# Kernel tuning notes

Hardware: AMD Instinct MI355X
Metric: run time of the kernel (lower is better)

The kernel has to match this reference:

```python
import jax, jax.numpy as jnp
import numpy as np

K = 1023   # kernel_size == embedding_dim
H = 16     # out_channels (filters per sample)
E = 256    # num_embeddings
T = 8      # num_tokens
CC = 0.25  # commitment cost
EPS = np.float32(np.finfo(np.float32).eps)
DN = ('NCH', 'OIH', 'NCH')


def setup_inputs() -> dict:
    key = jax.random.key(0)
    ks = jax.random.split(key, 10)
    B, C, L = 8, 1, 8184
    D_ff = 2 * E
    X = jax.random.normal(ks[0], (B, C, L), jnp.float32)
    embedding = jax.random.uniform(ks[1], (E, K), jnp.float32, -1.0 / E, 1.0 / E)
    ffn_w1 = jax.random.normal(ks[2], (E, D_ff), jnp.float32) * 0.02
    ffn_b1 = jnp.zeros((D_ff,), jnp.float32)
    ffn_w2 = jax.random.normal(ks[3], (D_ff, E), jnp.float32) * 0.02
    ffn_b2 = jnp.zeros((E,), jnp.float32)
    ln_g = jnp.ones((E,), jnp.float32)
    ln_b = jnp.zeros((E,), jnp.float32)
    cls_w = jax.random.normal(ks[4], (E, 10), jnp.float32) * 0.02
    cls_b = jnp.zeros((10,), jnp.float32)
    return dict(X=X, embedding=embedding, ffn_w1=ffn_w1, ffn_b1=ffn_b1,
                ffn_w2=ffn_w2, ffn_b2=ffn_b2, ln_g=ln_g, ln_b=ln_b,
                cls_w=cls_w, cls_b=cls_b)


def _autocov(f):
    # f: [..., K]. FFT-based autocovariance of hann-windowed, max-normalized frame.
    n = f.shape[-1]
    fmax = jnp.max(jnp.abs(f), axis=-1, keepdims=True)
    fmax = jnp.where(fmax == 0, EPS, fmax)
    win = 0.5 * (1.0 - jnp.cos(2.0 * jnp.pi * jnp.arange(n, dtype=jnp.float32) / n))
    xw = f * win / fmax
    spec = jnp.abs(jnp.fft.rfft(xw, n=n) ** 2)   # |rfft(x)^2| == |rfft(x)|^2
    return jnp.fft.ifftshift(jnp.fft.irfft(spec, n=n), axes=-1)


def reference(X, embedding, ffn_w1, ffn_b1, ffn_w2, ffn_b2, ln_g, ln_b, cls_w, cls_b):
    B, C, L = X.shape
    # ---- encoder: extract frames at fixed linspace positions, autocovariance ----
    Lp = ((L + K - 1) // K) * K          # PadForConv(zero) length (no-op here)
    end = Lp - K - 1 - K
    positions = jnp.linspace(0.0, float(end), H).astype(jnp.int32)
    idx = positions[:, None] + jnp.arange(K)          # (H, K)
    frames = X[:, :, idx]                             # (B, C, H, K) gather
    Z = _autocov(jnp.transpose(frames, (0, 2, 1, 3)))  # (B, H, C, K)
    # ---- VQ: pairwise distances + argmin + codebook lookup ----
    flat = Z.reshape(-1, K)                           # (B*H*C, K)
    d = (jnp.sum(flat ** 2, axis=1, keepdims=True)
         + jnp.sum(embedding ** 2, axis=1)
         - 2.0 * flat @ embedding.T)                  # (B*H*C, E)
    codes = jnp.argmin(d, axis=1)
    enc = jax.nn.one_hot(codes, E, dtype=flat.dtype)
    quant = (enc @ embedding).reshape(Z.shape)
    sg = jax.lax.stop_gradient
    e_loss = jnp.mean((sg(quant) - Z) ** 2)
    q_loss = jnp.mean((quant - sg(Z)) ** 2)
    vq_loss = q_loss + CC * e_loss
    quant_st = Z + sg(quant - Z)                      # straight-through
    avg = jnp.mean(enc, axis=0)
    perplexity = jnp.exp(-jnp.sum(avg * jnp.log(avg + EPS)))
    # ---- decoder: every sample's filter bank convolved with the whole batch ----
    fmerged = quant_st.reshape(B * H, C, K)           # merge per-sample banks
    out = jax.lax.conv_general_dilated(X, fmerged, (1,), 'SAME',
                                       dimension_numbers=DN)  # (B, B*H, L)
    out = out.reshape(B, B, H, L)                     # (batch b, filter-sample i, k, L)
    sq = (out - X[:, None, :, :]) ** 2                # C==1 broadcast
    # sum_i mean_k mse_{b,l} == mean over (b,k,l) then sum over i
    recon_loss = jnp.sum(jnp.mean(sq, axis=(0, 2, 3)))
    # ---- project: conv with codebook as filters ----
    pfilt = jnp.broadcast_to(embedding[:, None, :], (E, C, K))
    proj = jax.lax.conv_general_dilated(X, pfilt, (1,), 'VALID',
                                        dimension_numbers=DN)  # (B, E, Lo)
    Lo = proj.shape[-1]
    pad = ((Lo + T - 1) // T) * T - Lo                # PadForConv(mean)
    m = jnp.mean(proj, axis=-1, keepdims=True)
    proj = jnp.concatenate([proj, jnp.broadcast_to(m, (B, E, pad))], axis=-1)
    # ---- classify ----
    x = proj.reshape(B, E, T, -1).transpose(0, 2, 3, 1)  # (B, T, t, E)
    x = jnp.max(x, axis=2)                               # (B, T, E)
    mu = jnp.mean(x, axis=-1, keepdims=True)
    var = jnp.var(x, axis=-1, keepdims=True)
    xn = (x - mu) / jnp.sqrt(var + 1e-5) * ln_g + ln_b
    hdd = jax.nn.relu(xn @ ffn_w1 + ffn_b1) @ ffn_w2 + ffn_b2
    feat = jnp.mean(hdd, axis=1)                         # (B, E)
    logits = feat @ cls_w + cls_b
    return (logits, vq_loss, recon_loss, perplexity)
```

## Files before the change

kernel.cpp:

```cpp
#include <hip/hip_runtime.h>

#define KK 1023
#define LL 8184
#define LO 7162
#define XPS 10240
#define EPSF 1.1920928955078125e-07f
#define NEG_INF (-3.4028234663852886e+38f)

typedef short bf16x8 __attribute__((ext_vector_type(8)));
typedef float f32x4 __attribute__((ext_vector_type(4)));

__device__ __constant__ int c_pos[16] = {0,409,818,1227,1636,2045,2454,2863,
                                         3273,3682,4091,4500,4909,5318,5727,6137};

__device__ __forceinline__ unsigned short f2bf(float f) {
    unsigned u = __float_as_uint(f);
    unsigned r = (u + 0x7FFFu + ((u >> 16) & 1u)) >> 16;
    return (unsigned short)r;
}
__device__ __forceinline__ int fenc(float f) {
    int u = __float_as_int(f);
    return u >= 0 ? u : (~u) ^ 0x80000000;
}
__device__ __forceinline__ float fdec(int k) {
    int u = k >= 0 ? k : ~(k ^ 0x80000000);
    return __int_as_float(u);
}
__device__ __forceinline__ void gl2lds16(const void* g, void* l) {
    __builtin_amdgcn_global_load_lds(
        (const __attribute__((address_space(1))) void*)g,
        (__attribute__((address_space(3))) void*)l, 16, 0, 0);
}

__global__ __launch_bounds__(256) void k_prep(const float* __restrict__ X,
                                              const float* __restrict__ emb,
                                              unsigned short* __restrict__ Xpad,
                                              unsigned short* __restrict__ Xodd,
                                              unsigned short* __restrict__ Ebf,
                                              float* __restrict__ Etf,
                                              float* __restrict__ enorm,
                                              int* __restrict__ hist,
                                              int* __restrict__ cmax) {
    __shared__ float red[256];
    const int q = blockIdx.x;
    const int tid = threadIdx.x;
    if (q < 32) {
        const int b = q >> 2, seg = q & 3;
        for (int i = seg * 2560 + tid; i < (seg + 1) * 2560; i += 256) {
            unsigned short v = 0, vo = 0;
            if (i >= 512 && i < 512 + LL) v = f2bf(X[b * LL + (i - 512)]);
            const int i1 = i + 1;
            if (i1 >= 512 && i1 < 512 + LL) vo = f2bf(X[b * LL + (i1 - 512)]);
            Xpad[b * XPS + i] = v;
            Xodd[b * XPS + i] = vo;
        }
    } else if (q < 288) {
        const int e = q - 32;
        const float* er = emb + e * KK;
        float nrm = 0.f;
        for (int k = tid; k < 1024; k += 256) {
            float v = (k < KK) ? er[k] : 0.f;
            Ebf[e * 1024 + k] = (k < KK) ? f2bf(v) : (unsigned short)0;
            Etf[(k >> 2) * 1024 + e * 4 + (k & 3)] = v;
            nrm = fmaf(v, v, nrm);
        }
        red[tid] = nrm;
        __syncthreads();
        for (int off = 128; off; off >>= 1) {
            if (tid < off) red[tid] += red[tid + off];
            __syncthreads();
        }
        if (tid == 0) enorm[e] = red[0];
    } else {
        const int i = (q - 288) * 256 + tid;
        cmax[i] = INT_MIN;
        if (q == 288) hist[tid] = 0;
    }
}

__global__ __launch_bounds__(256) void k_autocov(const float* __restrict__ X,
                                                 float* __restrict__ Z) {
    __shared__ __align__(16) float xw[2046];
    __shared__ float red[256];
    const int fi = blockIdx.x >> 1, half = blockIdx.x & 1;
    const int b = fi >> 4, h = fi & 15;
    const int tid = threadIdx.x;
    const float* xp = X + b * LL + c_pos[h];

    float lmax = 0.f;
    for (int j = tid; j < KK; j += 256) {
        float v = xp[j];
        xw[j] = v;
        lmax = fmaxf(lmax, fabsf(v));
    }
    red[tid] = lmax;
    __syncthreads();
    for (int off = 128; off; off >>= 1) {
        if (tid < off) red[tid] = fmaxf(red[tid], red[tid + off]);
        __syncthreads();
    }
    float fmx = red[0];
    if (fmx == 0.f) fmx = EPSF;
    __syncthreads();
    for (int j = tid; j < KK; j += 256) {
        float v = xw[j];
        float win = 0.5f * (1.0f - cosf(6.28318530717958647692f * (float)j / 1023.0f));
        float w = v * win / fmx;
        xw[j] = w;
        xw[j + KK] = w;
    }
    __syncthreads();

    const int m2 = half * 512 + 2 * tid;
    const int mh = m2 >> 1;
    const float2* X2 = (const float2*)xw;
    float a0 = 0.f, a1 = 0.f;
    float2 F = X2[mh];
#pragma unroll 4
    for (int jh = 0; jh < 511; ++jh) {
        float2 xj = X2[jh];
        float2 G = X2[mh + jh + 1];
        a0 = fmaf(xj.x, F.x, a0);
        a0 = fmaf(xj.y, F.y, a0);
        a1 = fmaf(xj.x, F.y, a1);
        a1 = fmaf(xj.y, G.x, a1);
        F = G;
    }
    float xt = xw[1022];
    a0 = fmaf(xt, F.x, a0);
    a1 = fmaf(xt, F.y, a1);
    float* zrow = Z + fi * KK;
    int i0 = m2 + 512; if (i0 >= KK) i0 -= KK;
    zrow[i0] = a0;
    if (m2 + 1 < KK) {
        int i1 = m2 + 513; if (i1 >= KK) i1 -= KK;
        zrow[i1] = a1;
    }
}

__global__ __launch_bounds__(256) void k_vq(const float* __restrict__ Z,
                                            const float4* __restrict__ Et4,
                                            const float* __restrict__ enorm,
                                            const float* __restrict__ emb,
                                            int* __restrict__ codes,
                                            int* __restrict__ hist,
                                            float* __restrict__ vq_part) {
    __shared__ float zl[KK];
    __shared__ __align__(16) float zm2[1024];
    __shared__ float rv[256];
    __shared__ int   ri[256];
    const int fi = blockIdx.x, tid = threadIdx.x;
    const float* zrow = Z + fi * KK;
    for (int t = tid; t < 1024; t += 256) {
        float z = (t < KK) ? zrow[t] : 0.f;
        if (t < KK) zl[t] = z;
        zm2[t] = -2.f * z;
    }
    __syncthreads();

    float d = enorm[tid];
    const float4* zp = (const float4*)zm2;
    const float4* ep = Et4 + tid;
#pragma unroll 8
    for (int t4 = 0; t4 < 256; ++t4) {
        float4 ev = ep[t4 * 256];
        float4 zv = zp[t4];
        d = fmaf(zv.x, ev.x, d);
        d = fmaf(zv.y, ev.y, d);
        d = fmaf(zv.z, ev.z, d);
        d = fmaf(zv.w, ev.w, d);
    }
    rv[tid] = d; ri[tid] = tid;
    __syncthreads();
    for (int off = 128; off; off >>= 1) {
        if (tid < off) {
            float v2 = rv[tid + off]; int i2 = ri[tid + off];
            if (v2 < rv[tid] || (v2 == rv[tid] && i2 < ri[tid])) { rv[tid] = v2; ri[tid] = i2; }
        }
        __syncthreads();
    }
    const int code = ri[0];
    if (tid == 0) { codes[fi] = code; atomicAdd(&hist[code], 1); }

    const float* qr = emb + code * KK;
    float s = 0.f;
    for (int t = tid; t < KK; t += 256) { float dd = qr[t] - zl[t]; s += dd * dd; }
    __syncthreads();
    rv[tid] = s;
    __syncthreads();
    for (int off = 128; off; off >>= 1) {
        if (tid < off) rv[tid] += rv[tid + off];
        __syncthreads();
    }
    if (tid == 0) vq_part[fi] = rv[0];
}

__global__ __launch_bounds__(512, 6) void k_gemm(const unsigned short* __restrict__ Xpad,
                                                 const unsigned short* __restrict__ Xodd,
                                                 const unsigned short* __restrict__ Ebf,
                                                 const int* __restrict__ codes,
                                                 const float* __restrict__ X,
                                                 float* __restrict__ psum_part,
                                                 float* __restrict__ recon_part,
                                                 int* __restrict__ cmax) {
    __shared__ __align__(16) unsigned short lds_b[8 * 1280];
    __shared__ __align__(16) unsigned short lds_a[2 * 2048];
    __shared__ float red_s[64][4];
    const int tid  = threadIdx.x;
    const int lane = tid & 63;
    const int c = lane & 15, g = lane >> 4;
    const int w = tid >> 6, we = w & 1, wg = w >> 1;

    const int bi = blockIdx.x;
    const bool isproj = bi < 1024;
    int b, l0, row0;
    if (isproj) { b = bi >> 7; int r = bi & 127; row0 = (r >> 5) * 64; l0 = (r & 31) * 256; }
    else        { int q = bi - 1024; b = q >> 6; int r = q & 63; row0 = (r >> 5) * 64; l0 = (r & 31) * 256; }
    const int xw0 = (isproj ? 512 : 0) + l0;

    {
        const unsigned short* base_e = Xpad + b * XPS + xw0;
        const unsigned short* base_o = Xodd + b * XPS + xw0;
        for (int k = tid; k < 1280; k += 512) {
            const int wdw = k / 160;
            const int p = k - wdw * 160;
            const unsigned short* src = (wdw & 1) ? (base_o + wdw - 1 + p * 8)
                                                  : (base_e + wdw + p * 8);
            gl2lds16(src, lds_b + k * 8);
        }
    }
    const unsigned short* e_src = nullptr;
    if (tid < 256) {
        const int r_lds = tid >> 2, q4 = tid & 3;
        const int grow = isproj ? (row0 + r_lds) : codes[row0 + r_lds];
        e_src = Ebf + grow * 1024 + q4 * 8;
        gl2lds16(e_src, lds_a + tid * 8);
    }
    __syncthreads();

    f32x4 acc[2][4];
#pragma unroll
    for (int i = 0; i < 2; ++i)
#pragma unroll
        for (int j = 0; j < 4; ++j) acc[i][j] = (f32x4){0.f, 0.f, 0.f, 0.f};

    const char* lax = (const char*)lds_a;
    const char* lbx = (const char*)lds_b;
    const int boff0 = (wg & 1) * 10240 + ((wg >> 1) << 4) + 32 * c + 16 * g;
    const int aoff0 = (we * 32 + c) * 64 + g * 16;

    for (int s = 0; s < 32; ++s) {
        const int cur = s & 1;
        if (s + 1 < 32 && tid < 256)
            gl2lds16(e_src + (s + 1) * 32, lds_a + ((s + 1) & 1) * 2048 + tid * 8);
        const char* ab = lax + cur * 4096 + aoff0;
        bf16x8 af0 = *(const bf16x8*)(ab);
        bf16x8 af1 = *(const bf16x8*)(ab + 1024);
#pragma unroll
        for (int ntl = 0; ntl < 4; ++ntl) {
            bf16x8 bfrag = *(const bf16x8*)(lbx + boff0 + ntl * 2560 + 64 * s);
            acc[0][ntl] = __builtin_amdgcn_mfma_f32_16x16x32_bf16(af0, bfrag, acc[0][ntl], 0, 0, 0);
            acc[1][ntl] = __builtin_amdgcn_mfma_f32_16x16x32_bf16(af1, bfrag, acc[1][ntl], 0, 0, 0);
        }
        __syncthreads();
    }

    const int lseg  = l0 >> 8;
    const int lbase = l0 + wg * 4;
    if (isproj) {
        const int ch0 = lbase / 896;
#pragma unroll
        for (int et = 0; et < 2; ++et) {
#pragma unroll
            for (int r = 0; r < 4; ++r) {
                float ssum = 0.f, m0 = NEG_INF, m1 = NEG_INF;
#pragma unroll
                for (int ntl = 0; ntl < 4; ++ntl) {
                    float v = acc[et][ntl][r];
                    int l = lbase + ntl + 16 * c;
                    bool ok = l < LO;
                    ssum += ok ? v : 0.f;
                    int ch = l / 896;
                    if (ok && ch == ch0) m0 = fmaxf(m0, v);
                    if (ok && ch != ch0) m1 = fmaxf(m1, v);
                }
                ssum += __shfl_xor(ssum, 1); ssum += __shfl_xor(ssum, 2);
                ssum += __shfl_xor(ssum, 4); ssum += __shfl_xor(ssum, 8);
                m0 = fmaxf(m0, __shfl_xor(m0, 1)); m0 = fmaxf(m0, __shfl_xor(m0, 2));
                m0 = fmaxf(m0, __shfl_xor(m0, 4)); m0 = fmaxf(m0, __shfl_xor(m0, 8));
                m1 = fmaxf(m1, __shfl_xor(m1, 1)); m1 = fmaxf(m1, __shfl_xor(m1, 2));
                m1 = fmaxf(m1, __shfl_xor(m1, 4)); m1 = fmaxf(m1, __shfl_xor(m1, 8));
                if (c == 0) {
                    int eidx = we * 32 + et * 16 + g * 4 + r;
                    red_s[eidx][wg] = ssum;
                    int e = row0 + eidx;
                    int cb = (b * 256 + e) * 8;
                    if (m0 > NEG_INF && ch0 < 8)     atomicMax(&cmax[cb + ch0], fenc(m0));
                    if (m1 > NEG_INF && ch0 + 1 < 8) atomicMax(&cmax[cb + ch0 + 1], fenc(m1));
                }
            }
        }
    } else {
        float xv[4];
#pragma unroll
        for (int ntl = 0; ntl < 4; ++ntl) {
            int lr = lbase + ntl + 16 * c - 1;
            xv[ntl] = (lr >= 0 && lr < LL) ? X[b * LL + lr] : 0.f;
        }
#pragma unroll
        for (int et = 0; et < 2; ++et) {
#pragma unroll
            for (int r = 0; r < 4; ++r) {
                float ssum = 0.f;
#pragma unroll
                for (int ntl = 0; ntl < 4; ++ntl) {
                    int lr = lbase + ntl + 16 * c - 1;
                    bool ok = (lr >= 0) && (lr < LL);
                    float dd = ok ? (acc[et][ntl][r] - xv[ntl]) : 0.f;
                    ssum += dd * dd;
                }
                ssum += __shfl_xor(ssum, 1); ssum += __shfl_xor(ssum, 2);
                ssum += __shfl_xor(ssum, 4); ssum += __shfl_xor(ssum, 8);
                if (c == 0) red_s[we * 32 + et * 16 + g * 4 + r][wg] = ssum;
            }
        }
    }
    __syncthreads();
    if (tid < 64) {
        float tot = red_s[tid][0] + red_s[tid][1] + red_s[tid][2] + red_s[tid][3];
        if (isproj) {
            int e = row0 + tid;
            psum_part[lseg * 2048 + b * 256 + e] = tot;
        } else {
            int f = row0 + tid;
            recon_part[(b * 128 + f) * 32 + lseg] = tot;
        }
    }
}

__global__ __launch_bounds__(256) void k_ln(const float* __restrict__ psum_part,
                                            const int* __restrict__ cmax,
                                            const float* __restrict__ ln_g,
                                            const float* __restrict__ ln_b,
                                            float* __restrict__ xn) {
    __shared__ float red[256];
    __shared__ float red2[256];
    const int bt = blockIdx.x;
    const int t = bt & 7;
    const int b = bt >> 3;
    const int e = threadIdx.x;
    const float* ps = psum_part + b * 256 + e;
    float sm = 0.f;
#pragma unroll
    for (int s = 0; s < 32; ++s) sm += ps[s * 2048];
    float m = sm * (1.0f / 7162.0f);
    const int cb = (b * 256 + e) << 3;
    float v = (t < 7) ? fdec(cmax[cb + t]) : fmaxf(fdec(cmax[cb + 7]), m);
    red[e] = v; red2[e] = v * v;
    __syncthreads();
    for (int off = 128; off; off >>= 1) {
        if (e < off) { red[e] += red[e + off]; red2[e] += red2[e + off]; }
        __syncthreads();
    }
    float mu  = red[0] * (1.0f / 256.0f);
    float var = red2[0] * (1.0f / 256.0f) - mu * mu;
    float r = 1.0f / sqrtf(var + 1e-5f);
    xn[bt * 256 + e] = (v - mu) * r * ln_g[e] + ln_b[e];
}

__global__ __launch_bounds__(256) void k_ffn1(const float* __restrict__ xn,
                                              const float* __restrict__ w1,
                                              const float* __restrict__ b1,
                                              float* __restrict__ hbuf) {
    __shared__ float xr[256];
    __shared__ float rv[256];
    const int q = blockIdx.x;
    const int bt = q & 63, jc = q >> 6;
    const int tid = threadIdx.x;
    xr[tid] = xn[bt * 256 + tid];
    __syncthreads();
    const int jj = tid & 63, ks = tid >> 6;
    const int j = jc * 64 + jj;
    const float* wp = w1 + (ks * 64) * 512 + j;
    float a = 0.f;
#pragma unroll
    for (int ee = 0; ee < 64; ++ee) a = fmaf(xr[ks * 64 + ee], wp[ee * 512], a);
    rv[tid] = a;
    __syncthreads();
    if (tid < 64) {
        float s = rv[tid] + rv[tid + 64] + rv[tid + 128] + rv[tid + 192];
        hbuf[bt * 512 + jc * 64 + tid] = fmaxf(s + b1[jc * 64 + tid], 0.f);
    }
}

__global__ __launch_bounds__(256) void k_ffn2(const float* __restrict__ hbuf,
                                              const float* __restrict__ w2,
                                              const float* __restrict__ b2,
                                              float* __restrict__ hdd) {
    __shared__ float hr[512];
    __shared__ float rv[256];
    const int q = blockIdx.x;
    const int bt = q & 63, jc = q >> 6;
    const int tid = threadIdx.x;
    hr[tid] = hbuf[bt * 512 + tid];
    hr[tid + 256] = hbuf[bt * 512 + 256 + tid];
    __syncthreads();
    const int jj = tid & 63, ks = tid >> 6;
    const int e = jc * 64 + jj;
    const float* wp = w2 + (ks * 128) * 256 + e;
    float a = 0.f;
#pragma unroll
    for (int j = 0; j < 128; ++j) a = fmaf(hr[ks * 128 + j], wp[j * 256], a);
    rv[tid] = a;
    __syncthreads();
    if (tid < 64) {
        float s = rv[tid] + rv[tid + 64] + rv[tid + 128] + rv[tid + 192];
        hdd[bt * 256 + jc * 64 + tid] = s + b2[jc * 64 + tid];
    }
}

__global__ __launch_bounds__(256) void k_final(const float* __restrict__ hdd,
                                               const float* __restrict__ cls_w,
                                               const float* __restrict__ cls_b,
                                               const float* __restrict__ recon_part,
                                               const float* __restrict__ vq_part,
                                               const int* __restrict__ hist,
                                               float* __restrict__ out) {
    __shared__ float red[256];
    const int tid = threadIdx.x;
    if (blockIdx.x == 0) {
        __shared__ float feat[8][256];
#pragma unroll
        for (int b2 = 0; b2 < 8; ++b2) {
            float fb = 0.f;
#pragma unroll
            for (int t2 = 0; t2 < 8; ++t2) fb += hdd[(b2 * 8 + t2) * 256 + tid];
            feat[b2][tid] = fb * 0.125f;
        }
        __syncthreads();
        if (tid < 80) {
            const int b = tid / 10, k = tid % 10;
            float a = cls_b[k];
            for (int e = 0; e < 256; ++e) a = fmaf(feat[b][e], cls_w[e * 10 + k], a);
            out[tid] = a;
        }
    } else {
        float s = 0.f;
        for (int i = tid; i < 32768; i += 256) s += recon_part[i];
        red[tid] = s;
        __syncthreads();
        for (int off = 128; off; off >>= 1) { if (tid < off) red[tid] += red[tid + off]; __syncthreads(); }
        if (tid == 0) out[81] = red[0] / 1047552.0f;
        __syncthreads();
        red[tid] = (tid < 128) ? vq_part[tid] : 0.f;
        __syncthreads();
        for (int off = 128; off; off >>= 1) { if (tid < off) red[tid] += red[tid + off]; __syncthreads(); }
        if (tid == 0) out[80] = 1.25f * red[0] / 130944.0f;
        __syncthreads();
        float avg = (float)hist[tid] * (1.0f / 128.0f);
        red[tid] = avg * logf(avg + EPSF);
        __syncthreads();
        for (int off = 128; off; off >>= 1) { if (tid < off) red[tid] += red[tid + off]; __syncthreads(); }
        if (tid == 0) out[82] = expf(-red[0]);
    }
}

extern "C" void kernel_launch(void* const* d_in, const int* in_sizes, int n_in,
                              void* d_out, int out_size, void* d_ws, size_t ws_size,
                              hipStream_t stream) {
    const float* X     = (const float*)d_in[0];
    const float* emb   = (const float*)d_in[1];
    const float* w1    = (const float*)d_in[2];
    const float* b1    = (const float*)d_in[3];
    const float* w2    = (const float*)d_in[4];
    const float* b2    = (const float*)d_in[5];
    const float* ln_g  = (const float*)d_in[6];
    const float* ln_b  = (const float*)d_in[7];
    const float* cls_w = (const float*)d_in[8];
    const float* cls_b = (const float*)d_in[9];
    float* out = (float*)d_out;

    float* Z            = (float*)d_ws;
    float* vq_part      = Z + 130944;
    float* xnbuf        = vq_part + 128;
    float* hdd          = xnbuf + 16384;
    float* psum_part    = hdd + 16384;
    float* recon_part   = psum_part + 65536;
    int*   cmaxb        = (int*)(recon_part + 32768);
    int*   codes        = cmaxb + 16384;
    int*   hist         = codes + 128;
    unsigned short* Xpad = (unsigned short*)(hist + 256);
    unsigned short* Xodd = Xpad + 8 * XPS;
    unsigned short* Ebf  = Xodd + 8 * XPS;
    float* Etf           = (float*)(Ebf + 256 * 1024);
    float* enorm         = Etf + 256 * 1024;
    float* hbuf          = enorm + 256;

    k_prep   <<<dim3(352), dim3(256), 0, stream>>>(X, emb, Xpad, Xodd, Ebf, Etf, enorm, hist, cmaxb);
    k_autocov<<<dim3(256), dim3(256), 0, stream>>>(X, Z);
    k_vq     <<<dim3(128), dim3(256), 0, stream>>>(Z, (const float4*)Etf, enorm, emb, codes, hist, vq_part);
    k_gemm   <<<dim3(1536), dim3(512), 0, stream>>>(Xpad, Xodd, Ebf, codes, X, psum_part, recon_part, cmaxb);
    k_ln     <<<dim3(64),  dim3(256), 0, stream>>>(psum_part, cmaxb, ln_g, ln_b, xnbuf);
    k_ffn1   <<<dim3(512), dim3(256), 0, stream>>>(xnbuf, w1, b1, hbuf);
    k_ffn2   <<<dim3(256), dim3(256), 0, stream>>>(hbuf, w2, b2, hdd);
    k_final  <<<dim3(2),   dim3(256), 0, stream>>>(hdd, cls_w, cls_b, recon_part, vq_part, hist, out);
}
```

Baseline: 141.9 us.

## Merge autocov into prep kernel and give GEMM waves four row tiles

```diff
diff --git a/kernel.cpp b/kernel.cpp
--- a/kernel.cpp
+++ b/kernel.cpp
@@ -32,20 +32,91 @@
         (__attribute__((address_space(3))) void*)l, 16, 0, 0);
 }
 
-__global__ __launch_bounds__(256) void k_prep(const float* __restrict__ X,
-                                              const float* __restrict__ emb,
-                                              unsigned short* __restrict__ Xpad,
-                                              unsigned short* __restrict__ Xodd,
-                                              unsigned short* __restrict__ Ebf,
-                                              float* __restrict__ Etf,
-                                              float* __restrict__ enorm,
-                                              int* __restrict__ hist,
-                                              int* __restrict__ cmax) {
+__global__ __launch_bounds__(256) void k_pa(const float* __restrict__ X,
+                                            const float* __restrict__ emb,
+                                            unsigned short* __restrict__ Xpad,
+                                            unsigned short* __restrict__ Xodd,
+                                            unsigned short* __restrict__ Ebf,
+                                            float* __restrict__ Etf,
+                                            float* __restrict__ enorm,
+                                            int* __restrict__ hist,
+                                            int* __restrict__ cmax,
+                                            float* __restrict__ Z) {
+    __shared__ __align__(16) float xw[2046];
     __shared__ float red[256];
     const int q = blockIdx.x;
     const int tid = threadIdx.x;
-    if (q < 32) {
-        const int b = q >> 2, seg = q & 3;
+    if (q < 256) {
+        const int fi = q >> 1, half = q & 1;
+        const int b = fi >> 4, h = fi & 15;
+        const float* xp = X + b * LL + c_pos[h];
+        float lmax = 0.f;
+        for (int j = tid; j < KK; j += 256) {
+            float v = xp[j];
+            xw[j] = v;
+            lmax = fmaxf(lmax, fabsf(v));
+        }
+        red[tid] = lmax;
+        __syncthreads();
+        for (int off = 128; off; off >>= 1) {
+            if (tid < off) red[tid] = fmaxf(red[tid], red[tid + off]);
+            __syncthreads();
+        }
+        float fmx = red[0];
+        if (fmx == 0.f) fmx = EPSF;
+        __syncthreads();
+        for (int j = tid; j < KK; j += 256) {
+            float v = xw[j];
+            float win = 0.5f * (1.0f - cosf(6.28318530717958647692f * (float)j / 1023.0f));
+            float w = v * win / fmx;
+            xw[j] = w;
+            xw[j + KK] = w;
+        }
+        __syncthreads();
+
+        const int m2 = half * 512 + 2 * tid;
+        const int mh = m2 >> 1;
+        const float2* X2 = (const float2*)xw;
+        float a0 = 0.f, a1 = 0.f;
+        float2 F = X2[mh];
+#pragma unroll 2
+        for (int jh = 0; jh < 510; jh += 2) {
+            float2 xj0 = X2[jh];
+            float2 xj1 = X2[jh + 1];
+            float2 G0 = X2[mh + jh + 1];
+            float2 G1 = X2[mh + jh + 2];
+            a0 = fmaf(xj0.x, F.x, a0);
+            a0 = fmaf(xj0.y, F.y, a0);
+            a1 = fmaf(xj0.x, F.y, a1);
+            a1 = fmaf(xj0.y, G0.x, a1);
+            a0 = fmaf(xj1.x, G0.x, a0);
+            a0 = fmaf(xj1.y, G0.y, a0);
+            a1 = fmaf(xj1.x, G0.y, a1);
+            a1 = fmaf(xj1.y, G1.x, a1);
+            F = G1;
+        }
+        {
+            float2 xj = X2[510];
+            float2 G = X2[mh + 511];
+            a0 = fmaf(xj.x, F.x, a0);
+            a0 = fmaf(xj.y, F.y, a0);
+            a1 = fmaf(xj.x, F.y, a1);
+            a1 = fmaf(xj.y, G.x, a1);
+            F = G;
+        }
+        float xt = xw[1022];
+        a0 = fmaf(xt, F.x, a0);
+        a1 = fmaf(xt, F.y, a1);
+        float* zrow = Z + fi * KK;
+        int i0 = m2 + 512; if (i0 >= KK) i0 -= KK;
+        zrow[i0] = a0;
+        if (m2 + 1 < KK) {
+            int i1 = m2 + 513; if (i1 >= KK) i1 -= KK;
+            zrow[i1] = a1;
+        }
+    } else if (q < 288) {
+        const int qq = q - 256;
+        const int b = qq >> 2, seg = qq & 3;
         for (int i = seg * 2560 + tid; i < (seg + 1) * 2560; i += 256) {
             unsigned short v = 0, vo = 0;
             if (i >= 512 && i < 512 + LL) v = f2bf(X[b * LL + (i - 512)]);
@@ -54,8 +125,8 @@
             Xpad[b * XPS + i] = v;
             Xodd[b * XPS + i] = vo;
         }
-    } else if (q < 288) {
-        const int e = q - 32;
+    } else if (q < 544) {
+        const int e = q - 288;
         const float* er = emb + e * KK;
         float nrm = 0.f;
         for (int k = tid; k < 1024; k += 256) {
@@ -72,69 +143,9 @@
         }
         if (tid == 0) enorm[e] = red[0];
     } else {
-        const int i = (q - 288) * 256 + tid;
+        const int i = (q - 544) * 256 + tid;
         cmax[i] = INT_MIN;
-        if (q == 288) hist[tid] = 0;
-    }
-}
-
-__global__ __launch_bounds__(256) void k_autocov(const float* __restrict__ X,
-                                                 float* __restrict__ Z) {
-    __shared__ __align__(16) float xw[2046];
-    __shared__ float red[256];
-    const int fi = blockIdx.x >> 1, half = blockIdx.x & 1;
-    const int b = fi >> 4, h = fi & 15;
-    const int tid = threadIdx.x;
-    const float* xp = X + b * LL + c_pos[h];
-
-    float lmax = 0.f;
-    for (int j = tid; j < KK; j += 256) {
-        float v = xp[j];
-        xw[j] = v;
-        lmax = fmaxf(lmax, fabsf(v));
-    }
-    red[tid] = lmax;
-    __syncthreads();
-    for (int off = 128; off; off >>= 1) {
-        if (tid < off) red[tid] = fmaxf(red[tid], red[tid + off]);
-        __syncthreads();
-    }
-    float fmx = red[0];
-    if (fmx == 0.f) fmx = EPSF;
-    __syncthreads();
-    for (int j = tid; j < KK; j += 256) {
-        float v = xw[j];
-        float win = 0.5f * (1.0f - cosf(6.28318530717958647692f * (float)j / 1023.0f));
-        float w = v * win / fmx;
-        xw[j] = w;
-        xw[j + KK] = w;
-    }
-    __syncthreads();
-
-    const int m2 = half * 512 + 2 * tid;
-    const int mh = m2 >> 1;
-    const float2* X2 = (const float2*)xw;
-    float a0 = 0.f, a1 = 0.f;
-    float2 F = X2[mh];
-#pragma unroll 4
-    for (int jh = 0; jh < 511; ++jh) {
-        float2 xj = X2[jh];
-        float2 G = X2[mh + jh + 1];
-        a0 = fmaf(xj.x, F.x, a0);
-        a0 = fmaf(xj.y, F.y, a0);
-        a1 = fmaf(xj.x, F.y, a1);
-        a1 = fmaf(xj.y, G.x, a1);
-        F = G;
-    }
-    float xt = xw[1022];
-    a0 = fmaf(xt, F.x, a0);
-    a1 = fmaf(xt, F.y, a1);
-    float* zrow = Z + fi * KK;
-    int i0 = m2 + 512; if (i0 >= KK) i0 -= KK;
-    zrow[i0] = a0;
-    if (m2 + 1 < KK) {
-        int i1 = m2 + 513; if (i1 >= KK) i1 -= KK;
-        zrow[i1] = a1;
+        if (q == 544) hist[tid] = 0;
     }
 }
 
@@ -195,7 +206,7 @@
     if (tid == 0) vq_part[fi] = rv[0];
 }
 
-__global__ __launch_bounds__(512, 6) void k_gemm(const unsigned short* __restrict__ Xpad,
+__global__ __launch_bounds__(256, 4) void k_gemm(const unsigned short* __restrict__ Xpad,
                                                  const unsigned short* __restrict__ Xodd,
                                                  const unsigned short* __restrict__ Ebf,
                                                  const int* __restrict__ codes,
@@ -209,7 +220,7 @@
     const int tid  = threadIdx.x;
     const int lane = tid & 63;
     const int c = lane & 15, g = lane >> 4;
-    const int w = tid >> 6, we = w & 1, wg = w >> 1;
+    const int wg = tid >> 6;
 
     const int bi = blockIdx.x;
     const bool isproj = bi < 1024;
@@ -221,7 +232,7 @@
     {
         const unsigned short* base_e = Xpad + b * XPS + xw0;
         const unsigned short* base_o = Xodd + b * XPS + xw0;
-        for (int k = tid; k < 1280; k += 512) {
+        for (int k = tid; k < 1280; k += 256) {
             const int wdw = k / 160;
             const int p = k - wdw * 160;
             const unsigned short* src = (wdw & 1) ? (base_o + wdw - 1 + p * 8)
@@ -229,38 +240,37 @@
             gl2lds16(src, lds_b + k * 8);
         }
     }
-    const unsigned short* e_src = nullptr;
-    if (tid < 256) {
-        const int r_lds = tid >> 2, q4 = tid & 3;
-        const int grow = isproj ? (row0 + r_lds) : codes[row0 + r_lds];
-        e_src = Ebf + grow * 1024 + q4 * 8;
-        gl2lds16(e_src, lds_a + tid * 8);
-    }
-    __syncthreads();
-
-    f32x4 acc[2][4];
-#pragma unroll
-    for (int i = 0; i < 2; ++i)
+    const int r_lds = tid >> 2, q4 = tid & 3;
+    const int grow = isproj ? (row0 + r_lds) : codes[row0 + r_lds];
+    const unsigned short* e_src = Ebf + grow * 1024 + q4 * 8;
+    gl2lds16(e_src, lds_a + tid * 8);
+    __syncthreads();
+
+    f32x4 acc[4][4];
+#pragma unroll
+    for (int i = 0; i < 4; ++i)
 #pragma unroll
         for (int j = 0; j < 4; ++j) acc[i][j] = (f32x4){0.f, 0.f, 0.f, 0.f};
 
     const char* lax = (const char*)lds_a;
     const char* lbx = (const char*)lds_b;
     const int boff0 = (wg & 1) * 10240 + ((wg >> 1) << 4) + 32 * c + 16 * g;
-    const int aoff0 = (we * 32 + c) * 64 + g * 16;
+    const int aoff0 = c * 64 + g * 16;
 
     for (int s = 0; s < 32; ++s) {
         const int cur = s & 1;
-        if (s + 1 < 32 && tid < 256)
+        if (s + 1 < 32)
             gl2lds16(e_src + (s + 1) * 32, lds_a + ((s + 1) & 1) * 2048 + tid * 8);
         const char* ab = lax + cur * 4096 + aoff0;
-        bf16x8 af0 = *(const bf16x8*)(ab);
-        bf16x8 af1 = *(const bf16x8*)(ab + 1024);
+        bf16x8 af[4];
+#pragma unroll
+        for (int et = 0; et < 4; ++et) af[et] = *(const bf16x8*)(ab + et * 1024);
 #pragma unroll
         for (int ntl = 0; ntl < 4; ++ntl) {
             bf16x8 bfrag = *(const bf16x8*)(lbx + boff0 + ntl * 2560 + 64 * s);
-            acc[0][ntl] = __builtin_amdgcn_mfma_f32_16x16x32_bf16(af0, bfrag, acc[0][ntl], 0, 0, 0);
-            acc[1][ntl] = __builtin_amdgcn_mfma_f32_16x16x32_bf16(af1, bfrag, acc[1][ntl], 0, 0, 0);
+#pragma unroll
+            for (int et = 0; et < 4; ++et)
+                acc[et][ntl] = __builtin_amdgcn_mfma_f32_16x16x32_bf16(af[et], bfrag, acc[et][ntl], 0, 0, 0);
         }
         __syncthreads();
     }
@@ -270,7 +280,7 @@
     if (isproj) {
         const int ch0 = lbase / 896;
 #pragma unroll
-        for (int et = 0; et < 2; ++et) {
+        for (int et = 0; et < 4; ++et) {
 #pragma unroll
             for (int r = 0; r < 4; ++r) {
                 float ssum = 0.f, m0 = NEG_INF, m1 = NEG_INF;
@@ -291,7 +301,7 @@
                 m1 = fmaxf(m1, __shfl_xor(m1, 1)); m1 = fmaxf(m1, __shfl_xor(m1, 2));
                 m1 = fmaxf(m1, __shfl_xor(m1, 4)); m1 = fmaxf(m1, __shfl_xor(m1, 8));
                 if (c == 0) {
-                    int eidx = we * 32 + et * 16 + g * 4 + r;
+                    int eidx = et * 16 + g * 4 + r;
                     red_s[eidx][wg] = ssum;
                     int e = row0 + eidx;
                     int cb = (b * 256 + e) * 8;
@@ -308,7 +318,7 @@
             xv[ntl] = (lr >= 0 && lr < LL) ? X[b * LL + lr] : 0.f;
         }
 #pragma unroll
-        for (int et = 0; et < 2; ++et) {
+        for (int et = 0; et < 4; ++et) {
 #pragma unroll
             for (int r = 0; r < 4; ++r) {
                 float ssum = 0.f;
@@ -321,7 +331,7 @@
                 }
                 ssum += __shfl_xor(ssum, 1); ssum += __shfl_xor(ssum, 2);
                 ssum += __shfl_xor(ssum, 4); ssum += __shfl_xor(ssum, 8);
-                if (c == 0) red_s[we * 32 + et * 16 + g * 4 + r][wg] = ssum;
+                if (c == 0) red_s[et * 16 + g * 4 + r][wg] = ssum;
             }
         }
     }
@@ -496,10 +506,9 @@
     float* enorm         = Etf + 256 * 1024;
     float* hbuf          = enorm + 256;
 
-    k_prep   <<<dim3(352), dim3(256), 0, stream>>>(X, emb, Xpad, Xodd, Ebf, Etf, enorm, hist, cmaxb);
-    k_autocov<<<dim3(256), dim3(256), 0, stream>>>(X, Z);
+    k_pa     <<<dim3(608), dim3(256), 0, stream>>>(X, emb, Xpad, Xodd, Ebf, Etf, enorm, hist, cmaxb, Z);
     k_vq     <<<dim3(128), dim3(256), 0, stream>>>(Z, (const float4*)Etf, enorm, emb, codes, hist, vq_part);
-    k_gemm   <<<dim3(1536), dim3(512), 0, stream>>>(Xpad, Xodd, Ebf, codes, X, psum_part, recon_part, cmaxb);
+    k_gemm   <<<dim3(1536), dim3(256), 0, stream>>>(Xpad, Xodd, Ebf, codes, X, psum_part, recon_part, cmaxb);
     k_ln     <<<dim3(64),  dim3(256), 0, stream>>>(psum_part, cmaxb, ln_g, ln_b, xnbuf);
     k_ffn1   <<<dim3(512), dim3(256), 0, stream>>>(xnbuf, w1, b1, hbuf);
     k_ffn2   <<<dim3(256), dim3(256), 0, stream>>>(hbuf, w2, b2, hdd);
```

Measured after the change: 138.1 us. 2.7% less time.
